# Performance work log

Hardware: AMD Instinct MI355X
Metric: run time of the kernel (lower is better)

## Reference

```python
import jax, jax.numpy as jnp
import numpy as np

ALPHA = 0.2          # LeakyReLU negative slope (Alpha)
NEG_INF = -9e15      # mask value used by pygat-style GAT


def _masked_attention(Wh, a_src, a_dst, mask):
    """Wh: [H,N,d], a_src/a_dst: [H,d], mask: [N,N] (nonzero = edge).
    Returns attention-aggregated features [H,N,d]."""
    f_src = jnp.einsum('hnd,hd->hn', Wh, a_src)   # [H,N]
    f_dst = jnp.einsum('hnd,hd->hn', Wh, a_dst)   # [H,N]
    e = jax.nn.leaky_relu(f_src[:, :, None] + f_dst[:, None, :], ALPHA)  # [H,N,N]
    e = jnp.where(mask[None, :, :] > 0, e, NEG_INF)
    att = jax.nn.softmax(e, axis=-1)              # masked softmax over neighbors
    return jnp.einsum('hnm,hmd->hnd', att, Wh)    # [H,N,d]


def setup_inputs() -> dict:
    key = jax.random.key(0)
    ks = jax.random.split(key, 8)
    N, F_in, D, H = 4096, 512, 64, 8
    x = jax.random.normal(ks[0], (N, F_in), dtype=jnp.float32)
    adj = jax.random.randint(ks[1], (N, N), 0, 2, dtype=jnp.int32)
    s = 0.1
    W = jax.random.normal(ks[2], (H, F_in, D), dtype=jnp.float32) * s
    a_src = jax.random.normal(ks[3], (H, D), dtype=jnp.float32) * s
    a_dst = jax.random.normal(ks[4], (H, D), dtype=jnp.float32) * s
    W_o = jax.random.normal(ks[5], (H * D, D), dtype=jnp.float32) * s
    ao_src = jax.random.normal(ks[6], (D,), dtype=jnp.float32) * s
    ao_dst = jax.random.normal(ks[7], (D,), dtype=jnp.float32) * s
    return {"x": x, "adj": adj, "W": W, "a_src": a_src, "a_dst": a_dst,
            "W_o": W_o, "ao_src": ao_src, "ao_dst": ao_dst}


def reference(x, adj, W, a_src, a_dst, W_o, ao_src, ao_dst):
    N = x.shape[0]
    # --- multi-head layer (concat=True: ELU per head, concat on feature dim) ---
    Wh = jnp.einsum('nf,hfd->hnd', x, W)                     # [H,N,d]
    h1 = jax.nn.elu(_masked_attention(Wh, a_src, a_dst, adj))  # [H,N,d]
    h_cat = jnp.transpose(h1, (1, 0, 2)).reshape(N, -1)      # [N, H*d]
    # --- output head (concat=False: no ELU inside layer) ---
    Who = (h_cat @ W_o)[None]                                # [1,N,d]
    h2 = _masked_attention(Who, ao_src[None], ao_dst[None], adj)[0]  # [N,d]
    # GAT.forward: activation (ELU) then log_softmax over dim=1
    return jax.nn.log_softmax(jax.nn.elu(h2), axis=1)
```

## Files before the change

### kernel.cpp

```cpp
#include <hip/hip_runtime.h>
#include <hip/hip_bf16.h>
#include <math.h>

#define N_NODES 4096
#define FDIM 512
#define D 64
#define H 8
#define NWORDS (N_NODES / 64)

typedef __attribute__((ext_vector_type(8))) short bf16x8;
typedef __attribute__((ext_vector_type(4))) float f32x4;

__device__ inline short f2bf(float x) {
    return (short)((__builtin_bit_cast(unsigned int, x) + 0x8000u) >> 16);
}
__device__ inline float b2f(unsigned short s) {
    return __builtin_bit_cast(float, (unsigned int)s << 16);
}

__device__ inline int sext_bit(unsigned int v, int j) {
#if defined(__has_builtin) && __has_builtin(__builtin_amdgcn_sbfe)
    return __builtin_amdgcn_sbfe((int)v, j, 1);
#else
    return ((int)(v << (31 - j))) >> 31;
#endif
}

__device__ inline unsigned fenc(float f) {
    unsigned u = __builtin_bit_cast(unsigned, f);
    return (u & 0x80000000u) ? ~u : (u | 0x80000000u);
}
__device__ inline float fdec(unsigned e) {
    unsigned u = (e & 0x80000000u) ? (e & 0x7FFFFFFFu) : ~e;
    return __builtin_bit_cast(float, u);
}

__device__ inline void gl2lds16(const void* g, void* l) {
#if defined(__has_builtin) && __has_builtin(__builtin_amdgcn_global_load_lds)
    __builtin_amdgcn_global_load_lds(
        (const __attribute__((address_space(1))) unsigned int*)g,
        (__attribute__((address_space(3))) unsigned int*)l, 16, 0, 0);
#else
    *(uint4*)l = *(const uint4*)g;
#endif
}

#define NB_BITS (N_NODES * N_NODES / 2048)
#define NB_X    (N_NODES * FDIM / 1024)
#define NB_W    (H * FDIM * D / 256)
#define NB_WO   (FDIM * D / 256)
__global__ void k_pre(const int* __restrict__ adj, const float* __restrict__ x,
                      const float* __restrict__ W, const float* __restrict__ Wo,
                      unsigned int* __restrict__ bits32, short* __restrict__ Xbf,
                      short* __restrict__ WF, short* __restrict__ WoF,
                      float* __restrict__ cm1, float* __restrict__ cm2,
                      unsigned* __restrict__ gmaxe1, unsigned* __restrict__ gmaxe2) {
    const int b = blockIdx.x, t = threadIdx.x;
    if (b == 0) {
        for (int i = t; i < H * D; i += 256) cm1[i] = 0.f;
        if (t < D) cm2[t] = 0.f;
        if (t < H) gmaxe1[t] = 0u;
        if (t == 0) gmaxe2[0] = 0u;
        return;
    }
    if (b < 1 + NB_BITS) {
        const int tid  = (b - 1) * 256 + t;
        const size_t e0 = (size_t)tid * 8;
        int4 a0 = *(const int4*)&adj[e0];
        int4 a1 = *(const int4*)&adj[e0 + 4];
        unsigned by = (unsigned)(a0.x != 0)       | ((unsigned)(a0.y != 0) << 1)
                    | ((unsigned)(a0.z != 0) << 2) | ((unsigned)(a0.w != 0) << 3)
                    | ((unsigned)(a1.x != 0) << 4) | ((unsigned)(a1.y != 0) << 5)
                    | ((unsigned)(a1.z != 0) << 6) | ((unsigned)(a1.w != 0) << 7);
        unsigned v = by | (__shfl_xor((int)by, 1) << 8);
        v = v | ((unsigned)__shfl_xor((int)v, 2) << 16);
        if ((t & 3) == 0) bits32[tid >> 2] = v;
        return;
    }
    if (b < 1 + NB_BITS + NB_X) {
        const size_t i4 = ((size_t)(b - 1 - NB_BITS) * 256 + t) * 4;
        float4 v = *(const float4*)&x[i4];
        ushort4 o;
        o.x = (unsigned short)f2bf(v.x); o.y = (unsigned short)f2bf(v.y);
        o.z = (unsigned short)f2bf(v.z); o.w = (unsigned short)f2bf(v.w);
        *(ushort4*)&Xbf[i4] = o;
        return;
    }
    if (b < 1 + NB_BITS + NB_X + NB_W) {
        const size_t idx = (size_t)(b - 1 - NB_BITS - NB_X) * 256 + t;
        const int d = idx & 63;
        const int k = (int)(idx >> 6) & 511;
        const int h = (int)(idx >> 15);
        WF[(((size_t)h * 64 + (k >> 3)) * 64 + d) * 8 + (k & 7)] = f2bf(W[idx]);
        return;
    }
    {
        const size_t idx = (size_t)(b - 1 - NB_BITS - NB_X - NB_W) * 256 + t;
        const int d = idx & 63;
        const int k = (int)(idx >> 6);
        WoF[(((size_t)(k >> 3)) * 64 + d) * 8 + (k & 7)] = f2bf(Wo[idx]);
    }
}

__global__ void __launch_bounds__(256) k_gemm(
    const short* __restrict__ Xbf, const short* __restrict__ WF,
    const float* __restrict__ av, const float* __restrict__ bv,
    short* __restrict__ WBout, float* __restrict__ fs, float* __restrict__ fd,
    unsigned* __restrict__ gmaxe, float* __restrict__ cm) {
    const int h  = blockIdx.y;
    const int i0 = blockIdx.x * 64;
    const int t = threadIdx.x, w = t >> 6, lane = t & 63;
    const int li = lane & 15, quad = lane >> 4, k0 = quad * 8;
    const int row_a = i0 + w * 16 + li;
    const short* __restrict__ Xr  = Xbf + (size_t)row_a * FDIM;
    const short* __restrict__ WFh = WF + (size_t)h * 64 * D * 8;

    f32x4 c0 = {0.f, 0.f, 0.f, 0.f}, c1 = c0, c2 = c0, c3 = c0;
    #pragma unroll 4
    for (int kt = 0; kt < FDIM; kt += 32) {
        bf16x8 a = *(const bf16x8*)&Xr[kt + k0];
        const short* bb = WFh + (size_t)((kt >> 3) + quad) * (D * 8) + li * 8;
        bf16x8 b0 = *(const bf16x8*)(bb);
        bf16x8 b1 = *(const bf16x8*)(bb + 128);
        bf16x8 b2 = *(const bf16x8*)(bb + 256);
        bf16x8 b3 = *(const bf16x8*)(bb + 384);
        c0 = __builtin_amdgcn_mfma_f32_16x16x32_bf16(a, b0, c0, 0, 0, 0);
        c1 = __builtin_amdgcn_mfma_f32_16x16x32_bf16(a, b1, c1, 0, 0, 0);
        c2 = __builtin_amdgcn_mfma_f32_16x16x32_bf16(a, b2, c2, 0, 0, 0);
        c3 = __builtin_amdgcn_mfma_f32_16x16x32_bf16(a, b3, c3, 0, 0, 0);
    }
    float av4[4], bv4[4];
    #pragma unroll
    for (int t4 = 0; t4 < 4; ++t4) {
        av4[t4] = av[h * D + t4 * 16 + li];
        bv4[t4] = bv[h * D + t4 * 16 + li];
    }
    float tiles[4][4];
    #pragma unroll
    for (int r = 0; r < 4; ++r) { tiles[0][r] = c0[r]; tiles[1][r] = c1[r]; tiles[2][r] = c2[r]; tiles[3][r] = c3[r]; }

    __shared__ float csum[4][64];
    __shared__ float red[4];
    float fdmax = -INFINITY;
    float s4[4] = {0.f, 0.f, 0.f, 0.f};

    #pragma unroll
    for (int r = 0; r < 4; ++r) {
        const int row = i0 + w * 16 + quad * 4 + r;
        float pa = 0.f, pb = 0.f;
        #pragma unroll
        for (int t4 = 0; t4 < 4; ++t4) {
            const float v = tiles[t4][r];
            const int d = t4 * 16 + li;
            WBout[((size_t)h * (N_NODES / 8) + (row >> 3)) * (D * 8) + d * 8 + (row & 7)] = f2bf(v);
            pa += v * av4[t4];
            pb += v * bv4[t4];
            s4[t4] += v;
        }
        #pragma unroll
        for (int off = 1; off < 16; off <<= 1) {
            pa += __shfl_xor(pa, off);
            pb += __shfl_xor(pb, off);
        }
        if (li == 0) {
            fs[(size_t)h * N_NODES + row] = pa;
            fd[(size_t)h * N_NODES + row] = pb;
        }
        fdmax = fmaxf(fdmax, pb);
    }
    fdmax = fmaxf(fdmax, __shfl_xor(fdmax, 16));
    fdmax = fmaxf(fdmax, __shfl_xor(fdmax, 32));
    if (lane == 0) red[w] = fdmax;
    #pragma unroll
    for (int t4 = 0; t4 < 4; ++t4) {
        s4[t4] += __shfl_xor(s4[t4], 16);
        s4[t4] += __shfl_xor(s4[t4], 32);
    }
    if (quad == 0)
        #pragma unroll
        for (int t4 = 0; t4 < 4; ++t4) csum[w][t4 * 16 + li] = s4[t4];
    __syncthreads();
    if (t == 0)
        atomicMax(gmaxe + h, fenc(fmaxf(fmaxf(red[0], red[1]), fmaxf(red[2], red[3]))));
    if (t < 64)
        atomicAdd(&cm[h * D + t],
                  (csum[0][t] + csum[1][t] + csum[2][t] + csum[3][t]) * (1.f / (float)N_NODES));
}

__global__ void __launch_bounds__(256) k_accum(
    const unsigned int* __restrict__ bits32,
    const short* __restrict__ WB,
    const float* __restrict__ fsb, const float* __restrict__ fdb,
    const unsigned* __restrict__ gmaxe,
    short* __restrict__ num, float* __restrict__ den, int kslab) {

    __shared__ __align__(16) short Bt[2][16 * 64 * 8];
    __shared__ __align__(16) float EG[2][256];

    const int h = blockIdx.y, i0 = blockIdx.x * 256, slab = blockIdx.z;
    const int t = threadIdx.x, w = t >> 6, lane = t & 63;
    const int li = lane & 15, quad = lane >> 4, k0 = quad * 8;
    const size_t ho = (size_t)h * N_NODES;
    const float  gm = fdec(gmaxe[h]);
    float Rv[4];
    const unsigned int* __restrict__ brow[4];
    #pragma unroll
    for (int f = 0; f < 4; ++f) {
        const int r = i0 + w * 64 + f * 16 + li;
        Rv[f] = __expf(-0.8f * (fsb[ho + r] + gm));
        brow[f] = bits32 + (size_t)r * (NWORDS * 2);
    }
    const float* __restrict__ fd = fdb + ho;
    const short* __restrict__ Bh = WB + (size_t)h * (N_NODES / 8) * D * 8;

    f32x4 acc[4][4], c5[4];
    #pragma unroll
    for (int f = 0; f < 4; ++f) {
        #pragma unroll
        for (int q = 0; q < 4; ++q) acc[f][q] = (f32x4){0.f, 0.f, 0.f, 0.f};
        c5[f] = (f32x4){0.f, 0.f, 0.f, 0.f};
    }
    bf16x8 ones;
    #pragma unroll
    for (int j = 0; j < 8; ++j) ones[j] = (short)0x3F80;

    const int k_beg = slab * kslab;
    const int ntile = kslab / 128;

    auto stage = [&](int buf, int jt) {
        const short* src = Bh + (size_t)(jt >> 3) * (D * 8);
        #pragma unroll
        for (int p = 0; p < 4; ++p)
            gl2lds16(src + (size_t)(p * 256 + t) * 8, &Bt[buf][(p * 256 + t) * 8]);
        if (w == 0) {
            float2 f2 = *(const float2*)&fd[jt + lane * 2];
            float2 ev, gv;
            ev.x = __expf(f2.x - gm);          ev.y = __expf(f2.y - gm);
            gv.x = __expf(0.2f * (f2.x - gm)); gv.y = __expf(0.2f * (f2.y - gm));
            *(float2*)&EG[buf][lane * 2]       = ev;
            *(float2*)&EG[buf][128 + lane * 2] = gv;
        }
    };

    stage(0, k_beg);
    uint4 bw[4];
    #pragma unroll
    for (int f = 0; f < 4; ++f) bw[f] = *(const uint4*)&brow[f][k_beg >> 5];
    for (int tile = 0; tile < ntile; ++tile) {
        const int jt = k_beg + tile * 128;
        __syncthreads();
        if (tile + 1 < ntile) stage((tile + 1) & 1, jt + 128);
        const short* Bl  = Bt[tile & 1];
        const float* EGl = EG[tile & 1];
        unsigned int bwa[4][4];
        #pragma unroll
        for (int f = 0; f < 4; ++f) {
            bwa[f][0] = bw[f].x; bwa[f][1] = bw[f].y; bwa[f][2] = bw[f].z; bwa[f][3] = bw[f].w;
        }
        if (tile + 1 < ntile)
            #pragma unroll
            for (int f = 0; f < 4; ++f) bw[f] = *(const uint4*)&brow[f][(jt + 128) >> 5];
        #pragma unroll
        for (int s = 0; s < 4; ++s) {
            const float4 e0 = *(const float4*)&EGl[s * 32 + k0];
            const float4 e1 = *(const float4*)&EGl[s * 32 + k0 + 4];
            const float4 g0 = *(const float4*)&EGl[128 + s * 32 + k0];
            const float4 g1 = *(const float4*)&EGl[128 + s * 32 + k0 + 4];
            float ev[8], gv[8];
            ev[0] = e0.x; ev[1] = e0.y; ev[2] = e0.z; ev[3] = e0.w;
            ev[4] = e1.x; ev[5] = e1.y; ev[6] = e1.z; ev[7] = e1.w;
            gv[0] = g0.x; gv[1] = g0.y; gv[2] = g0.z; gv[3] = g0.w;
            gv[4] = g1.x; gv[5] = g1.y; gv[6] = g1.z; gv[7] = g1.w;
            const short* bb = Bl + (size_t)((s * 4 + quad) * 64 + li) * 8;
            bf16x8 b0 = *(const bf16x8*)(bb);
            bf16x8 b1 = *(const bf16x8*)(bb + 128);
            bf16x8 b2 = *(const bf16x8*)(bb + 256);
            bf16x8 b3 = *(const bf16x8*)(bb + 384);
            #pragma unroll
            for (int f = 0; f < 4; ++f) {
                const unsigned int byt = (bwa[f][s] >> k0) & 0xFFu;
                unsigned int pa[8];
                #pragma unroll
                for (int j = 0; j < 8; ++j) {
                    const float p = fmaxf(ev[j], gv[j] * Rv[f]);
                    pa[j] = __builtin_bit_cast(unsigned int, p)
                            & (unsigned int)sext_bit(byt, j);
                }
                bf16x8 a;
                unsigned int* au = (unsigned int*)&a;
                au[0] = __builtin_amdgcn_perm(pa[1], pa[0], 0x07060302);
                au[1] = __builtin_amdgcn_perm(pa[3], pa[2], 0x07060302);
                au[2] = __builtin_amdgcn_perm(pa[5], pa[4], 0x07060302);
                au[3] = __builtin_amdgcn_perm(pa[7], pa[6], 0x07060302);
                acc[f][0] = __builtin_amdgcn_mfma_f32_16x16x32_bf16(a, b0, acc[f][0], 0, 0, 0);
                acc[f][1] = __builtin_amdgcn_mfma_f32_16x16x32_bf16(a, b1, acc[f][1], 0, 0, 0);
                acc[f][2] = __builtin_amdgcn_mfma_f32_16x16x32_bf16(a, b2, acc[f][2], 0, 0, 0);
                acc[f][3] = __builtin_amdgcn_mfma_f32_16x16x32_bf16(a, b3, acc[f][3], 0, 0, 0);
                c5[f]     = __builtin_amdgcn_mfma_f32_16x16x32_bf16(a, ones, c5[f], 0, 0, 0);
            }
        }
    }

    const size_t so = (size_t)(slab * gridDim.y + h);
    #pragma unroll
    for (int f = 0; f < 4; ++f) {
        #pragma unroll
        for (int t4 = 0; t4 < 4; ++t4)
            #pragma unroll
            for (int r = 0; r < 4; ++r) {
                const int row = i0 + w * 64 + f * 16 + quad * 4 + r;
                num[(so * N_NODES + row) * D + t4 * 16 + li] = f2bf(acc[f][t4][r]);
            }
        if (li == 0)
            #pragma unroll
            for (int r = 0; r < 4; ++r)
                den[so * N_NODES + i0 + w * 64 + f * 16 + quad * 4 + r] = c5[f][r];
    }
}

__global__ void k_post1(const short* __restrict__ num, const float* __restrict__ den,
                        const float* __restrict__ colmean, short* __restrict__ hcat) {
    const int h   = blockIdx.y;
    const int i0  = blockIdx.x * 64;
    const int t   = threadIdx.x;
    const int row = i0 + (t >> 2);
    const int cb  = (t & 3) * 16;
    const size_t HN = (size_t)gridDim.y * N_NODES;
    const size_t r0 = (size_t)h * N_NODES + row;
    float dsum = 0.f;
    #pragma unroll
    for (int s = 0; s < 8; ++s) dsum += den[s * HN + r0];
    const bool  uni  = !(dsum > 0.f);
    const float linv = uni ? 0.f : 1.f / dsum;
    #pragma unroll
    for (int c = 0; c < 4; ++c) {
        const int col = cb + c * 4;
        float4 v = {0.f, 0.f, 0.f, 0.f};
        #pragma unroll
        for (int s = 0; s < 8; ++s) {
            ushort4 a = *(const ushort4*)&num[(s * HN + r0) * D + col];
            v.x += b2f(a.x); v.y += b2f(a.y); v.z += b2f(a.z); v.w += b2f(a.w);
        }
        v.x *= linv; v.y *= linv; v.z *= linv; v.w *= linv;
        if (uni) v = *(const float4*)&colmean[h * D + col];
        v.x = v.x > 0.f ? v.x : __expf(v.x) - 1.f;
        v.y = v.y > 0.f ? v.y : __expf(v.y) - 1.f;
        v.z = v.z > 0.f ? v.z : __expf(v.z) - 1.f;
        v.w = v.w > 0.f ? v.w : __expf(v.w) - 1.f;
        ushort4 o;
        o.x = (unsigned short)f2bf(v.x); o.y = (unsigned short)f2bf(v.y);
        o.z = (unsigned short)f2bf(v.z); o.w = (unsigned short)f2bf(v.w);
        *(ushort4*)&hcat[(size_t)row * (H * D) + h * D + col] = o;
    }
}

__global__ void k_lsm(const short* __restrict__ num, const float* __restrict__ den,
                      const float* __restrict__ cm, float* __restrict__ out) {
    const int n    = blockIdx.x * 4 + (threadIdx.x >> 6);
    const int lane = threadIdx.x & 63;
    float v = 0.f, ds = 0.f;
    #pragma unroll
    for (int s = 0; s < 32; ++s)
        v += b2f((unsigned short)num[((size_t)s * N_NODES + n) * D + lane]);
    #pragma unroll
    for (int s = 0; s < 32; ++s) ds += den[(size_t)s * N_NODES + n];
    v = (ds > 0.f) ? v / ds : cm[lane];
    v = v > 0.f ? v : __expf(v) - 1.f;
    float mx = v;
    #pragma unroll
    for (int off = 32; off > 0; off >>= 1) mx = fmaxf(mx, __shfl_xor(mx, off));
    float ex = __expf(v - mx);
    float sum = ex;
    #pragma unroll
    for (int off = 32; off > 0; off >>= 1) sum += __shfl_xor(sum, off);
    out[(size_t)n * D + lane] = (v - mx) - __logf(sum);
}

extern "C" void kernel_launch(void* const* d_in, const int* in_sizes, int n_in,
                              void* d_out, int out_size, void* d_ws, size_t ws_size,
                              hipStream_t stream) {
    const float* x      = (const float*)d_in[0];
    const int*   adj    = (const int*)d_in[1];
    const float* W      = (const float*)d_in[2];
    const float* a_src  = (const float*)d_in[3];
    const float* a_dst  = (const float*)d_in[4];
    const float* W_o    = (const float*)d_in[5];
    const float* ao_src = (const float*)d_in[6];
    const float* ao_dst = (const float*)d_in[7];
    float* out = (float*)d_out;

    char* wsp = (char*)d_ws;
    size_t off = 0;
    auto alloc = [&](size_t bytes) -> void* {
        void* p = wsp + off;
        off += (bytes + 255) & ~(size_t)255;
        return p;
    };
    unsigned* adj_bits = (unsigned*)alloc((size_t)N_NODES * NWORDS * 8);
    short*    Xbf   = (short*)alloc((size_t)N_NODES * FDIM * 2);
    short*    WF1   = (short*)alloc((size_t)H * 64 * D * 8 * 2);
    short*    WoF   = (short*)alloc((size_t)64 * D * 8 * 2);
    short*    WhB   = (short*)alloc((size_t)H * N_NODES * D * 2);
    float*    fs1   = (float*)alloc((size_t)H * N_NODES * 4);
    float*    fd1   = (float*)alloc((size_t)H * N_NODES * 4);
    unsigned* gme1  = (unsigned*)alloc((size_t)H * 4);
    float*    cm1   = (float*)alloc((size_t)H * D * 4);
    short*    num1  = (short*)alloc((size_t)8 * H * N_NODES * D * 2);
    float*    den1  = (float*)alloc((size_t)8 * H * N_NODES * 4);
    short*    hcat  = (short*)alloc((size_t)N_NODES * H * D * 2);
    short*    WhoB  = (short*)alloc((size_t)N_NODES * D * 2);
    float*    fs2   = (float*)alloc((size_t)N_NODES * 4);
    float*    fd2   = (float*)alloc((size_t)N_NODES * 4);
    unsigned* gme2  = (unsigned*)alloc(4);
    float*    cm2   = (float*)alloc((size_t)D * 4);
    short*    num2  = (short*)alloc((size_t)32 * N_NODES * D * 2);
    float*    den2  = (float*)alloc((size_t)32 * N_NODES * 4);

    k_pre  <<<dim3(1 + NB_BITS + NB_X + NB_W + NB_WO), dim3(256), 0, stream>>>(
        adj, x, W, W_o, adj_bits, Xbf, WF1, WoF, cm1, cm2, gme1, gme2);

    k_gemm <<<dim3(N_NODES / 64, H), dim3(256), 0, stream>>>(Xbf, WF1, a_src, a_dst,
                                                             WhB, fs1, fd1, gme1, cm1);
    k_accum<<<dim3(N_NODES / 256, H, 8), dim3(256), 0, stream>>>(adj_bits, WhB, fs1, fd1, gme1,
                                                                 num1, den1, N_NODES / 8);
    k_post1<<<dim3(N_NODES / 64, H), dim3(256), 0, stream>>>(num1, den1, cm1, hcat);

    k_gemm <<<dim3(N_NODES / 64, 1), dim3(256), 0, stream>>>(hcat, WoF, ao_src, ao_dst,
                                                             WhoB, fs2, fd2, gme2, cm2);
    k_accum<<<dim3(N_NODES / 256, 1, 32), dim3(256), 0, stream>>>(adj_bits, WhoB, fs2, fd2, gme2,
                                                                  num2, den2, N_NODES / 32);
    k_lsm  <<<dim3(N_NODES / 4), dim3(256), 0, stream>>>(num2, den2, cm2, out);
}
```

Baseline: 203.5 us.

## Load B fragments directly from global memory in k_accum, drop LDS staging

Removes the double-buffered LDS staging of the B tile (global_load_lds) and the per-tile __syncthreads. Each wave now reads its B fragments straight from global memory (relying on L1/L2 hits) and computes its own EG exp values into a private per-wave LDS slice. Launch bounds also request 4 blocks per SIMD-occupancy. This trades LDS traffic and barriers for redundant global loads, the loss of prefetch overlap, and four waves repeating the exp computation.

```diff
diff --git a/kernel.cpp b/kernel.cpp
--- a/kernel.cpp
+++ b/kernel.cpp
@@ -33,16 +33,6 @@
 __device__ inline float fdec(unsigned e) {
     unsigned u = (e & 0x80000000u) ? (e & 0x7FFFFFFFu) : ~e;
     return __builtin_bit_cast(float, u);
-}
-
-__device__ inline void gl2lds16(const void* g, void* l) {
-#if defined(__has_builtin) && __has_builtin(__builtin_amdgcn_global_load_lds)
-    __builtin_amdgcn_global_load_lds(
-        (const __attribute__((address_space(1))) unsigned int*)g,
-        (__attribute__((address_space(3))) unsigned int*)l, 16, 0, 0);
-#else
-    *(uint4*)l = *(const uint4*)g;
-#endif
 }
 
 #define NB_BITS (N_NODES * N_NODES / 2048)
@@ -187,15 +177,14 @@
                   (csum[0][t] + csum[1][t] + csum[2][t] + csum[3][t]) * (1.f / (float)N_NODES));
 }
 
-__global__ void __launch_bounds__(256) k_accum(
+__global__ void __launch_bounds__(256, 4) k_accum(
     const unsigned int* __restrict__ bits32,
     const short* __restrict__ WB,
     const float* __restrict__ fsb, const float* __restrict__ fdb,
     const unsigned* __restrict__ gmaxe,
     short* __restrict__ num, float* __restrict__ den, int kslab) {
 
-    __shared__ __align__(16) short Bt[2][16 * 64 * 8];
-    __shared__ __align__(16) float EG[2][256];
+    __shared__ __align__(16) float EG[4][256];
 
     const int h = blockIdx.y, i0 = blockIdx.x * 256, slab = blockIdx.z;
     const int t = threadIdx.x, w = t >> 6, lane = t & 63;
@@ -212,6 +201,7 @@
     }
     const float* __restrict__ fd = fdb + ho;
     const short* __restrict__ Bh = WB + (size_t)h * (N_NODES / 8) * D * 8;
+    float* __restrict__ EGw = EG[w];
 
     f32x4 acc[4][4], c5[4];
     #pragma unroll
@@ -224,54 +214,37 @@
     #pragma unroll
     for (int j = 0; j < 8; ++j) ones[j] = (short)0x3F80;
 
-    const int k_beg = slab * kslab;
-    const int ntile = kslab / 128;
-
-    auto stage = [&](int buf, int jt) {
-        const short* src = Bh + (size_t)(jt >> 3) * (D * 8);
-        #pragma unroll
-        for (int p = 0; p < 4; ++p)
-            gl2lds16(src + (size_t)(p * 256 + t) * 8, &Bt[buf][(p * 256 + t) * 8]);
-        if (w == 0) {
+    const int k_beg = slab * kslab, k_end = k_beg + kslab;
+
+    for (int jt = k_beg; jt < k_end; jt += 128) {
+        {
             float2 f2 = *(const float2*)&fd[jt + lane * 2];
             float2 ev, gv;
             ev.x = __expf(f2.x - gm);          ev.y = __expf(f2.y - gm);
             gv.x = __expf(0.2f * (f2.x - gm)); gv.y = __expf(0.2f * (f2.y - gm));
-            *(float2*)&EG[buf][lane * 2]       = ev;
-            *(float2*)&EG[buf][128 + lane * 2] = gv;
-        }
-    };
-
-    stage(0, k_beg);
-    uint4 bw[4];
-    #pragma unroll
-    for (int f = 0; f < 4; ++f) bw[f] = *(const uint4*)&brow[f][k_beg >> 5];
-    for (int tile = 0; tile < ntile; ++tile) {
-        const int jt = k_beg + tile * 128;
-        __syncthreads();
-        if (tile + 1 < ntile) stage((tile + 1) & 1, jt + 128);
-        const short* Bl  = Bt[tile & 1];
-        const float* EGl = EG[tile & 1];
+            *(float2*)&EGw[lane * 2]       = ev;
+            *(float2*)&EGw[128 + lane * 2] = gv;
+        }
+        uint4 bw[4];
+        #pragma unroll
+        for (int f = 0; f < 4; ++f) bw[f] = *(const uint4*)&brow[f][jt >> 5];
         unsigned int bwa[4][4];
         #pragma unroll
         for (int f = 0; f < 4; ++f) {
             bwa[f][0] = bw[f].x; bwa[f][1] = bw[f].y; bwa[f][2] = bw[f].z; bwa[f][3] = bw[f].w;
         }
-        if (tile + 1 < ntile)
-            #pragma unroll
-            for (int f = 0; f < 4; ++f) bw[f] = *(const uint4*)&brow[f][(jt + 128) >> 5];
         #pragma unroll
         for (int s = 0; s < 4; ++s) {
-            const float4 e0 = *(const float4*)&EGl[s * 32 + k0];
-            const float4 e1 = *(const float4*)&EGl[s * 32 + k0 + 4];
-            const float4 g0 = *(const float4*)&EGl[128 + s * 32 + k0];
-            const float4 g1 = *(const float4*)&EGl[128 + s * 32 + k0 + 4];
+            const float4 e0 = *(const float4*)&EGw[s * 32 + k0];
+            const float4 e1 = *(const float4*)&EGw[s * 32 + k0 + 4];
+            const float4 g0 = *(const float4*)&EGw[128 + s * 32 + k0];
+            const float4 g1 = *(const float4*)&EGw[128 + s * 32 + k0 + 4];
             float ev[8], gv[8];
             ev[0] = e0.x; ev[1] = e0.y; ev[2] = e0.z; ev[3] = e0.w;
             ev[4] = e1.x; ev[5] = e1.y; ev[6] = e1.z; ev[7] = e1.w;
             gv[0] = g0.x; gv[1] = g0.y; gv[2] = g0.z; gv[3] = g0.w;
             gv[4] = g1.x; gv[5] = g1.y; gv[6] = g1.z; gv[7] = g1.w;
-            const short* bb = Bl + (size_t)((s * 4 + quad) * 64 + li) * 8;
+            const short* bb = Bh + (size_t)(((jt + s * 32) >> 3) + quad) * (D * 8) + li * 8;
             bf16x8 b0 = *(const bf16x8*)(bb);
             bf16x8 b1 = *(const bf16x8*)(bb + 128);
             bf16x8 b2 = *(const bf16x8*)(bb + 256);
```

After: 359.9 us. +76.8%, slower.
